# Kernel tuning notes

Measured on AMD Instinct MI355X. Metric: run time of the kernel, lower is better.

Reference implementation:

```python
import jax, jax.numpy as jnp
import numpy as np

NUM_TREES = 100
VOCAB = 100000
DIM = 32            # dim_leaf_emb
ATT = DIM // 2      # att_dim = 16
BS = 1024

# pair indices matching itertools.combinations(range(n), 2)
_ROW, _COL = np.triu_indices(NUM_TREES, k=1)


def setup_inputs() -> dict:
    key = jax.random.key(0)
    ks = jax.random.split(key, 12)
    x = jax.random.randint(ks[0], (BS, NUM_TREES), 0, VOCAB)
    Emb = jax.random.normal(ks[1], (VOCAB, DIM), dtype=jnp.float32) * 0.02
    W = jax.random.normal(ks[2], (DIM, ATT), dtype=jnp.float32) * (1.0 / np.sqrt(DIM))
    b = jnp.zeros((ATT,), dtype=jnp.float32)
    h = jax.random.normal(ks[3], (ATT,), dtype=jnp.float32) * 0.1
    W1 = jax.random.normal(ks[4], (DIM, DIM // 2), dtype=jnp.float32) * (1.0 / np.sqrt(DIM))
    b1 = jnp.zeros((DIM // 2,), dtype=jnp.float32)
    W2 = jax.random.normal(ks[5], (DIM // 2, DIM // 4), dtype=jnp.float32) * (1.0 / np.sqrt(DIM // 2))
    b2 = jnp.zeros((DIM // 4,), dtype=jnp.float32)
    Wf = jax.random.normal(ks[6], (DIM // 4, 1), dtype=jnp.float32) * (1.0 / np.sqrt(DIM // 4))
    bf = jnp.zeros((1,), dtype=jnp.float32)
    return {"x": x, "Emb": Emb, "W": W, "b": b, "h": h,
            "W1": W1, "b1": b1, "W2": W2, "b2": b2, "Wf": Wf, "bf": bf}


def reference(x, Emb, W, b, h, W1, b1, W2, b2, Wf, bf):
    e = Emb[x]                                   # (bs, T, D)
    half_bip = e[:, _ROW] * e[:, _COL]           # (bs, P, D), P = T*(T-1)/2
    s = jax.nn.relu(jnp.einsum('bpd,da->bpa', half_bip, W) + b)  # (bs, P, A)
    att = jax.nn.softmax(jnp.einsum('bpa,a->bp', s, h), axis=-1) # (bs, P)
    pooled = jnp.einsum('bpd,bp->bd', half_bip, att)             # (bs, D)
    o = jax.nn.relu(pooled @ W1 + b1)
    o = jax.nn.relu(o @ W2 + b2)
    return jax.nn.sigmoid(o @ Wf + bf)           # (bs, 1)
```

## Files before the change

kernel.cpp:

```cpp
#include <hip/hip_runtime.h>
#include <math.h>

constexpr int kT = 100;
constexpr int kP = 4950;
constexpr int kD = 32;
constexpr int kA = 16;
constexpr int kESH = 40;
constexpr int kTiles = (kP + 15) / 16;
constexpr int kTblPad = 4960;
constexpr int kNT = 512;

typedef float    float4v __attribute__((ext_vector_type(4)));
typedef __fp16   fp16x2  __attribute__((ext_vector_type(2)));
typedef __fp16   half4   __attribute__((ext_vector_type(4)));
typedef __fp16   half8   __attribute__((ext_vector_type(8)));
typedef _Float16 half8v  __attribute__((ext_vector_type(8)));

__device__ __forceinline__ void pair_decode(int p, int& r, int& c) {
    const float tq = 39601.0f - 8.0f * (float)p;
    r = (int)((199.0f - sqrtf(tq)) * 0.5f);
    if (r < 0) r = 0;
    if (r > 98) r = 98;
    int base = r * 99 - ((r * (r - 1)) >> 1);
    while (base > p) { --r; base = r * 99 - ((r * (r - 1)) >> 1); }
    while (p - base >= (99 - r)) { base += (99 - r); ++r; }
    c = r + 1 + (p - base);
}

__global__ void pair_init(unsigned int* __restrict__ tbl) {
    const int p = blockIdx.x * 256 + threadIdx.x;
    if (p < kTblPad) {
        int r, c;
        pair_decode(p < kP ? p : kP - 1, r, c);
        tbl[p] = ((unsigned)(r * kESH * 2) << 16) | (unsigned)(c * kESH * 2);
    }
}

template <bool USE_TBL>
__global__ __launch_bounds__(kNT, 8)
void afm_kernel(const int* __restrict__ x,
                const float* __restrict__ Emb,
                const float* __restrict__ W,
                const float* __restrict__ bb,
                const float* __restrict__ h,
                const float* __restrict__ W1,
                const float* __restrict__ b1,
                const float* __restrict__ W2,
                const float* __restrict__ b2,
                const float* __restrict__ Wf,
                const float* __restrict__ bf,
                const unsigned int* __restrict__ tbl,
                float* __restrict__ out)
{
    __shared__ __align__(16) unsigned char smem[27840];
    __shared__ float red[8];
    __shared__ float sh_pooled[kD];
    __shared__ float sh_o1[kA];
    __shared__ float sh_o2[8];

    __fp16* she = (__fp16*)smem;
    unsigned int* sh_tbl = (unsigned int*)(smem + 8000);

    const int tid  = threadIdx.x;
    const int b    = blockIdx.x;
    const int lane = tid & 63;
    const int wv   = tid >> 6;
    const int quad = lane >> 4;
    const int l15  = lane & 15;
    const int k0   = quad * 8;

    const int* xb = x + b * kT;
    for (int i = tid; i < kT * 8; i += kNT) {
        const int row = i >> 3, c4 = i & 7;
        const int v = xb[row];
        const float4 val = ((const float4*)Emb)[v * 8 + c4];
        union { fp16x2 h2[2]; half4 h4; } tmp;
        tmp.h2[0] = __builtin_amdgcn_cvt_pkrtz(val.x, val.y);
        tmp.h2[1] = __builtin_amdgcn_cvt_pkrtz(val.z, val.w);
        *(half4*)(she + row * kESH + c4 * 4) = tmp.h4;
    }
    if (USE_TBL) {
        const uint4* t4 = (const uint4*)tbl;
        for (int i = tid; i < kTblPad / 4; i += kNT)
            ((uint4*)sh_tbl)[i] = t4[i];
    } else {
        for (int p = tid; p < kTblPad; p += kNT) {
            int r, c;
            pair_decode(p < kP ? p : kP - 1, r, c);
            sh_tbl[p] = ((unsigned)(r * kESH * 2) << 16) | (unsigned)(c * kESH * 2);
        }
    }

    union { fp16x2 h2[4]; half8v h8; } wa;
#pragma unroll
    for (int j = 0; j < 4; ++j)
        wa.h2[j] = __builtin_amdgcn_cvt_pkrtz(W[(k0 + 2 * j) * kA + l15],
                                              W[(k0 + 2 * j + 1) * kA + l15]);
    float h_reg[4];
    float4v bfrag;
#pragma unroll
    for (int rg = 0; rg < 4; ++rg) {
        h_reg[rg] = h[quad * 4 + rg] * 1.44269504088896340736f;
        bfrag[rg] = bb[quad * 4 + rg];
    }
    const char* sheq = (const char*)she + k0 * 2;
    __syncthreads();

    float pool[8];
#pragma unroll
    for (int j = 0; j < 8; ++j) pool[j] = 0.0f;
    float lsum = 0.0f;

#pragma unroll 4
    for (int t = wv; t < kTiles; t += 8) {
        const int p_raw = t * 16 + l15;
        const unsigned pr = sh_tbl[p_raw];

        const half8 er = *(const half8*)(sheq + (pr >> 16));
        const half8 ec = *(const half8*)(sheq + (pr & 0xFFFFu));
        union { half8 fp; half8v mf; } hb;
        hb.fp = er * ec;

        float4v acc = __builtin_amdgcn_mfma_f32_16x16x32_f16(wa.h8, hb.mf, bfrag, 0, 0, 0);

        float part = 0.0f;
#pragma unroll
        for (int rg = 0; rg < 4; ++rg)
            part = fmaf(fmaxf(acc[rg], 0.0f), h_reg[rg], part);
        part += __shfl_xor(part, 16, 64);
        part += __shfl_xor(part, 32, 64);

        const float w = (p_raw < kP) ? exp2f(part) : 0.0f;
        lsum += w;
#pragma unroll
        for (int j = 0; j < 8; ++j)
            pool[j] = fmaf(w, (float)hb.fp[j], pool[j]);
    }

#pragma unroll
    for (int off = 1; off < 64; off <<= 1) lsum += __shfl_xor(lsum, off, 64);
    if (lane == 0) red[wv] = lsum;

    __syncthreads();
    float* stg = (float*)smem;
#pragma unroll
    for (int j = 0; j < 8; ++j) stg[tid * 9 + j] = pool[j];
    __syncthreads();

    if (tid < kD) {
        const float invS = 4.0f / (red[0] + red[1] + red[2] + red[3] +
                                   red[4] + red[5] + red[6] + red[7]);
        const int q = tid >> 3, j = tid & 7;
        float s = 0.0f;
        for (int w8 = 0; w8 < 8; ++w8)
            for (int l = 0; l < 16; ++l)
                s += stg[(w8 * 64 + q * 16 + l) * 9 + j];
        sh_pooled[tid] = s * invS;
    }
    __syncthreads();

    if (tid < kA) {
        float o = b1[tid];
#pragma unroll
        for (int d = 0; d < kD; ++d) o = fmaf(sh_pooled[d], W1[d * kA + tid], o);
        sh_o1[tid] = fmaxf(o, 0.0f);
    }
    __syncthreads();
    if (tid < 8) {
        float o = b2[tid];
#pragma unroll
        for (int a = 0; a < kA; ++a) o = fmaf(sh_o1[a], W2[a * 8 + tid], o);
        sh_o2[tid] = fmaxf(o, 0.0f);
    }
    __syncthreads();
    if (tid == 0) {
        float z = bf[0];
#pragma unroll
        for (int j = 0; j < 8; ++j) z = fmaf(sh_o2[j], Wf[j], z);
        out[b] = 1.0f / (1.0f + __expf(-z));
    }
}

extern "C" void kernel_launch(void* const* d_in, const int* in_sizes, int n_in,
                              void* d_out, int out_size, void* d_ws, size_t ws_size,
                              hipStream_t stream) {
    const int*   x   = (const int*)d_in[0];
    const float* Emb = (const float*)d_in[1];
    const float* W   = (const float*)d_in[2];
    const float* bb  = (const float*)d_in[3];
    const float* h   = (const float*)d_in[4];
    const float* W1  = (const float*)d_in[5];
    const float* b1  = (const float*)d_in[6];
    const float* W2  = (const float*)d_in[7];
    const float* b2  = (const float*)d_in[8];
    const float* Wf  = (const float*)d_in[9];
    const float* bf  = (const float*)d_in[10];
    float* out = (float*)d_out;

    if (ws_size >= (size_t)(kTblPad * 4)) {
        unsigned int* tbl = (unsigned int*)d_ws;
        pair_init<<<(kTblPad + 255) / 256, 256, 0, stream>>>(tbl);
        afm_kernel<true><<<1024, kNT, 0, stream>>>(x, Emb, W, bb, h, W1, b1, W2, b2,
                                                   Wf, bf, tbl, out);
    } else {
        afm_kernel<false><<<1024, kNT, 0, stream>>>(x, Emb, W, bb, h, W1, b1, W2, b2,
                                                    Wf, bf, nullptr, out);
    }
}
```

Before: 115.6 us.

## Iterate pairs row-by-row without pair table, pool in packed fp16

Removes the precomputed pair index table and the separate pair_init launch. Each wave now walks whole rows of the upper-triangular pair set, reusing the row embedding in registers across 16-column tiles. Rows are assigned in a balanced pattern, and 16 zero-padded embedding rows make the masked tail-tile reads safe. Pooling accumulators switch to packed fp16 and exp2 uses the hardware builtin, which cuts per-tile ALU work but may lose precision when accumulating many weighted products in half precision.

```diff
diff --git a/kernel.cpp b/kernel.cpp
--- a/kernel.cpp
+++ b/kernel.cpp
@@ -2,12 +2,10 @@
 #include <math.h>
 
 constexpr int kT = 100;
-constexpr int kP = 4950;
 constexpr int kD = 32;
 constexpr int kA = 16;
 constexpr int kESH = 40;
-constexpr int kTiles = (kP + 15) / 16;
-constexpr int kTblPad = 4960;
+constexpr int kRows = 116;
 constexpr int kNT = 512;
 
 typedef float    float4v __attribute__((ext_vector_type(4)));
@@ -16,27 +14,12 @@
 typedef __fp16   half8   __attribute__((ext_vector_type(8)));
 typedef _Float16 half8v  __attribute__((ext_vector_type(8)));
 
-__device__ __forceinline__ void pair_decode(int p, int& r, int& c) {
-    const float tq = 39601.0f - 8.0f * (float)p;
-    r = (int)((199.0f - sqrtf(tq)) * 0.5f);
-    if (r < 0) r = 0;
-    if (r > 98) r = 98;
-    int base = r * 99 - ((r * (r - 1)) >> 1);
-    while (base > p) { --r; base = r * 99 - ((r * (r - 1)) >> 1); }
-    while (p - base >= (99 - r)) { base += (99 - r); ++r; }
-    c = r + 1 + (p - base);
-}
+#if __has_builtin(__builtin_amdgcn_exp2f)
+#define EXP2F(x) __builtin_amdgcn_exp2f(x)
+#else
+#define EXP2F(x) exp2f(x)
+#endif
 
-__global__ void pair_init(unsigned int* __restrict__ tbl) {
-    const int p = blockIdx.x * 256 + threadIdx.x;
-    if (p < kTblPad) {
-        int r, c;
-        pair_decode(p < kP ? p : kP - 1, r, c);
-        tbl[p] = ((unsigned)(r * kESH * 2) << 16) | (unsigned)(c * kESH * 2);
-    }
-}
-
-template <bool USE_TBL>
 __global__ __launch_bounds__(kNT, 8)
 void afm_kernel(const int* __restrict__ x,
                 const float* __restrict__ Emb,
@@ -49,17 +32,16 @@
                 const float* __restrict__ b2,
                 const float* __restrict__ Wf,
                 const float* __restrict__ bf,
-                const unsigned int* __restrict__ tbl,
                 float* __restrict__ out)
 {
-    __shared__ __align__(16) unsigned char smem[27840];
+    __shared__ __align__(16) unsigned char smem[18432];
     __shared__ float red[8];
     __shared__ float sh_pooled[kD];
     __shared__ float sh_o1[kA];
     __shared__ float sh_o2[8];
 
     __fp16* she = (__fp16*)smem;
-    unsigned int* sh_tbl = (unsigned int*)(smem + 8000);
+    const char* sheb = (const char*)smem;
 
     const int tid  = threadIdx.x;
     const int b    = blockIdx.x;
@@ -79,17 +61,8 @@
         tmp.h2[1] = __builtin_amdgcn_cvt_pkrtz(val.z, val.w);
         *(half4*)(she + row * kESH + c4 * 4) = tmp.h4;
     }
-    if (USE_TBL) {
-        const uint4* t4 = (const uint4*)tbl;
-        for (int i = tid; i < kTblPad / 4; i += kNT)
-            ((uint4*)sh_tbl)[i] = t4[i];
-    } else {
-        for (int p = tid; p < kTblPad; p += kNT) {
-            int r, c;
-            pair_decode(p < kP ? p : kP - 1, r, c);
-            sh_tbl[p] = ((unsigned)(r * kESH * 2) << 16) | (unsigned)(c * kESH * 2);
-        }
-    }
+    if (tid < (kRows - kT) * kESH / 2)
+        ((unsigned int*)she)[kT * kESH / 2 + tid] = 0u;
 
     union { fp16x2 h2[4]; half8v h8; } wa;
 #pragma unroll
@@ -103,39 +76,52 @@
         h_reg[rg] = h[quad * 4 + rg] * 1.44269504088896340736f;
         bfrag[rg] = bb[quad * 4 + rg];
     }
-    const char* sheq = (const char*)she + k0 * 2;
+    const int lane_base = l15 * 80 + quad * 16;
     __syncthreads();
 
-    float pool[8];
+    fp16x2 pool2[4];
+    const fp16x2 zz = {(__fp16)0.0f, (__fp16)0.0f};
 #pragma unroll
-    for (int j = 0; j < 8; ++j) pool[j] = 0.0f;
+    for (int j = 0; j < 4; ++j) pool2[j] = zz;
     float lsum = 0.0f;
 
-#pragma unroll 4
-    for (int t = wv; t < kTiles; t += 8) {
-        const int p_raw = t * 16 + l15;
-        const unsigned pr = sh_tbl[p_raw];
+    union HB { half8 fp; fp16x2 h2[4]; half8v mf; };
 
-        const half8 er = *(const half8*)(sheq + (pr >> 16));
-        const half8 ec = *(const half8*)(sheq + (pr & 0xFFFFu));
-        union { half8 fp; half8v mf; } hb;
-        hb.fp = er * ec;
-
+    auto do_tile = [&](const half8& er, int coff, int rem, bool mask) {
+        HB hb;
+        hb.fp = er * (*(const half8*)(sheb + coff));
         float4v acc = __builtin_amdgcn_mfma_f32_16x16x32_f16(wa.h8, hb.mf, bfrag, 0, 0, 0);
-
         float part = 0.0f;
 #pragma unroll
         for (int rg = 0; rg < 4; ++rg)
             part = fmaf(fmaxf(acc[rg], 0.0f), h_reg[rg], part);
         part += __shfl_xor(part, 16, 64);
         part += __shfl_xor(part, 32, 64);
+        float w = EXP2F(part);
+        if (mask) w = (l15 < rem) ? w : 0.0f;
+        lsum += w;
+        const fp16x2 ww = __builtin_amdgcn_cvt_pkrtz(w, w);
+#pragma unroll
+        for (int j = 0; j < 4; ++j)
+            pool2[j] += ww * hb.h2[j];
+    };
 
-        const float w = (p_raw < kP) ? exp2f(part) : 0.0f;
-        lsum += w;
-#pragma unroll
-        for (int j = 0; j < 8; ++j)
-            pool[j] = fmaf(w, (float)hb.fp[j], pool[j]);
+    auto do_row = [&](int r) {
+        const int len = 99 - r;
+        const int nfull = (len - 1) >> 4;
+        const half8 er = *(const half8*)(sheb + r * 80 + quad * 16);
+        int coff = (r + 1) * 80 + lane_base;
+        for (int j = 0; j < nfull; ++j, coff += 1280)
+            do_tile(er, coff, 16, false);
+        do_tile(er, coff, len - (nfull << 4), true);
+    };
+
+    for (int g = 0; g < 6; ++g) {
+        const int wvg = (wv + g) & 7;
+        do_row(g * 16 + wvg);
+        do_row(g * 16 + 15 - wvg);
     }
+    if (wv < 3) do_row(96 + wv);
 
 #pragma unroll
     for (int off = 1; off < 64; off <<= 1) lsum += __shfl_xor(lsum, off, 64);
@@ -144,7 +130,10 @@
     __syncthreads();
     float* stg = (float*)smem;
 #pragma unroll
-    for (int j = 0; j < 8; ++j) stg[tid * 9 + j] = pool[j];
+    for (int j = 0; j < 4; ++j) {
+        stg[tid * 9 + 2 * j]     = (float)pool2[j][0];
+        stg[tid * 9 + 2 * j + 1] = (float)pool2[j][1];
+    }
     __syncthreads();
 
     if (tid < kD) {
@@ -197,13 +186,5 @@
     const float* bf  = (const float*)d_in[10];
     float* out = (float*)d_out;
 
-    if (ws_size >= (size_t)(kTblPad * 4)) {
-        unsigned int* tbl = (unsigned int*)d_ws;
-        pair_init<<<(kTblPad + 255) / 256, 256, 0, stream>>>(tbl);
-        afm_kernel<true><<<1024, kNT, 0, stream>>>(x, Emb, W, bb, h, W1, b1, W2, b2,
-                                                   Wf, bf, tbl, out);
-    } else {
-        afm_kernel<false><<<1024, kNT, 0, stream>>>(x, Emb, W, bb, h, W1, b1, W2, b2,
-                                                    Wf, bf, nullptr, out);
-    }
+    afm_kernel<<<1024, kNT, 0, stream>>>(x, Emb, W, bb, h, W1, b1, W2, b2, Wf, bf, out);
 }
```

After: 107.0 us. -7.4%, faster.
